# Optimization experiments

Hardware: AMD Instinct MI355X
Metric: run time of the kernel (lower is better)

## Reference

```python
import jax, jax.numpy as jnp
import numpy as np

WS = 25          # window_size
THRESHOLD = 3.5  # default threshold in find_low_quality_regions


def _conv1d_gelu(x, w, b, pad):
    # x: (N, C_in, L), w: (C_out, C_in, K) -> gelu(conv(x) + b), SAME length
    y = jax.lax.conv_general_dilated(
        x, w, window_strides=(1,), padding=[(pad, pad)],
        dimension_numbers=("NCH", "OIH", "NCH"))
    return jax.nn.gelu(y + b[None, :, None], approximate=False)


def setup_inputs() -> dict:
    key = jax.random.key(0)
    ks = jax.random.split(key, 12)
    B, T, D, H = 8, 25000, 256, 128
    s = 0.05
    return {
        "latents": jax.random.normal(ks[0], (B, T, D), jnp.float32),
        "conv0_w": jax.random.normal(ks[1], (H, D, 7), jnp.float32) * s,
        "conv0_b": jax.random.normal(ks[2], (H,), jnp.float32) * s,
        "conv1_w": jax.random.normal(ks[3], (H, H, 5), jnp.float32) * s,
        "conv1_b": jax.random.normal(ks[4], (H,), jnp.float32) * s,
        "conv2_w": jax.random.normal(ks[5], (H, H, 5), jnp.float32) * s,
        "conv2_b": jax.random.normal(ks[6], (H,), jnp.float32) * s,
        "head_w1": jax.random.normal(ks[7], (H, H), jnp.float32) * s,
        "head_b1": jax.random.normal(ks[8], (H,), jnp.float32) * s,
        "head_w2": jax.random.normal(ks[9], (1, H), jnp.float32) * s,
        "head_b2": jax.random.normal(ks[10], (1,), jnp.float32) * s,
    }


def reference(latents, conv0_w, conv0_b, conv1_w, conv1_b, conv2_w, conv2_b,
              head_w1, head_b1, head_w2, head_b2):
    B, T, D = latents.shape
    nw = (T - WS) // WS + 1  # number of non-overlapping windows
    # (B, nw, WS, D) -> (B*nw, D, WS): batch all windows through the critic
    x = latents[:, :nw * WS].reshape(B, nw, WS, D).reshape(B * nw, WS, D)
    x = jnp.transpose(x, (0, 2, 1))  # NCH
    x = _conv1d_gelu(x, conv0_w, conv0_b, pad=3)
    x = _conv1d_gelu(x, conv1_w, conv1_b, pad=2)
    x = _conv1d_gelu(x, conv2_w, conv2_b, pad=2)
    feat = x.mean(axis=2)  # AdaptiveAvgPool1d(1) -> (B*nw, H)
    h = jax.nn.gelu(feat @ head_w1.T + head_b1, approximate=False)
    score = jax.nn.sigmoid(h @ head_w2.T + head_b2)[:, 0] * 5.0  # (B*nw,)
    scores = score.reshape(B, nw).mean(axis=0)  # critic(window).mean() per window
    low_quality = scores < THRESHOLD  # windows the loop would append as regions
    return scores, low_quality
```

## Files before the change

### kernel.cpp

```cpp
#include <hip/hip_runtime.h>
#include <math.h>

#define BATCH 8
#define T_LEN 25000
#define NW    1000
#define WS    25
#define D0    256
#define H     128

typedef __bf16 bf16;
typedef bf16 bf16x8 __attribute__((ext_vector_type(8)));
typedef bf16 bf16x4 __attribute__((ext_vector_type(4)));
typedef float f32x4 __attribute__((ext_vector_type(4)));

__device__ __forceinline__ float gelu_fast(float x) {
    float y = 0.7978845608f * x * (1.0f + 0.044715f * x * x);
    float e = __expf(2.0f * y);
    float t = 1.0f - 2.0f * __builtin_amdgcn_rcpf(e + 1.0f);
    return 0.5f * x * (1.0f + t);
}

__global__ void repack_w(const float* __restrict__ w, bf16* __restrict__ dst,
                         int Cin, int K, int KSn, int total) {
    int t = blockIdx.x * 256 + threadIdx.x;
    if (t >= total) return;
    int j    = t & 7;
    int lane = (t >> 3) & 63;
    int mt   = (t >> 9) & 7;
    int ks   = (t >> 12) % KSn;
    int k    = t / (4096 * KSn);
    int m = lane & 15, q = lane >> 4;
    int co = mt * 16 + m;
    int ci = ks * 32 + q * 8 + j;
    dst[t] = (bf16)w[(co * Cin + ci) * K + k];
}

__global__ void cvt_bf16(const float* __restrict__ w, bf16* __restrict__ dst, int n) {
    int t = blockIdx.x * 256 + threadIdx.x;
    if (t < n) dst[t] = (bf16)w[t];
}

#define XT_LD 264
#define A_LD  136
#define OFF_A1   16896
#define OFF_FEAT 24784
#define OFF_H    25296
#define SMEM_BYTES 27200

__global__ __launch_bounds__(256, 6)
void critic_kernel(const float* __restrict__ lat,
                   const bf16* __restrict__ p0, const float* __restrict__ b0,
                   const bf16* __restrict__ p1, const float* __restrict__ b1,
                   const bf16* __restrict__ p2, const float* __restrict__ b2,
                   const bf16* __restrict__ hw1b, const float* __restrict__ hb1,
                   const float* __restrict__ hw2, const float* __restrict__ hb2,
                   float* __restrict__ scores_tmp) {
    __shared__ __align__(16) char smem[SMEM_BYTES];
    bf16  (*xT)[XT_LD]  = (bf16(*)[XT_LD])smem;
    bf16  (*a2T)[A_LD]  = (bf16(*)[A_LD])smem;
    bf16  (*a1T)[A_LD]  = (bf16(*)[A_LD])(smem + OFF_A1);
    float* feat = (float*)(smem + OFF_FEAT);
    float* hbuf = (float*)(smem + OFF_H);

    const int tid = threadIdx.x;
    const int bx  = blockIdx.x;
    const int b   = bx / NW;
    const int w   = bx % NW;

    {
        const float4* src4 = (const float4*)(lat + ((size_t)b * T_LEN + (size_t)w * WS) * D0);
        #pragma unroll
        for (int it = 0; it < 7; ++it) {
            int g = tid + it * 256;
            if (g < 1600) {
                int l = g >> 6, c0 = (g & 63) * 4;
                float4 v = src4[g];
                bf16x4 o = {(bf16)v.x, (bf16)v.y, (bf16)v.z, (bf16)v.w};
                *(bf16x4*)&xT[l + 3][c0] = o;
            }
        }
        bf16x4 z4 = {};
        #pragma unroll
        for (int it = 0; it < 2; ++it) {
            int i = tid + it * 256;
            if (i < 448) {
                int rr = i >> 6;
                int r = (rr < 3) ? rr : rr + 25;
                *(bf16x4*)&xT[r][(i & 63) * 4] = z4;
            }
        }
        {
            if (tid < 128) {
                int rr = tid >> 5;
                int r = (rr < 2) ? rr : rr + 25;
                *(bf16x4*)&a1T[r][(tid & 31) * 4] = z4;
            }
        }
    }
    __syncthreads();

    const int lane = tid & 63, wv = tid >> 6;
    const int m = lane & 15, q = lane >> 4;
    const bf16* xbase  = &xT[m][q * 8];
    const bf16* a1base = &a1T[m][q * 8];

    f32x4 acc[2][2] = {};
    {
        const bf16x8* A = (const bf16x8*)p0 + (size_t)wv * 64 + lane;
        #pragma unroll
        for (int k = 0; k < 7; ++k) {
            #pragma unroll
            for (int ks = 0; ks < 8; ++ks) {
                bf16x8 a0 = A[(k * 8 + ks) * 512];
                bf16x8 a1 = A[(k * 8 + ks) * 512 + 256];
                bf16x8 bb0 = *(const bf16x8*)(xbase + k * XT_LD + ks * 32);
                bf16x8 bb1 = *(const bf16x8*)(xbase + k * XT_LD + ks * 32 + 16 * XT_LD);
                acc[0][0] = __builtin_amdgcn_mfma_f32_16x16x32_bf16(a0, bb0, acc[0][0], 0, 0, 0);
                acc[0][1] = __builtin_amdgcn_mfma_f32_16x16x32_bf16(a0, bb1, acc[0][1], 0, 0, 0);
                acc[1][0] = __builtin_amdgcn_mfma_f32_16x16x32_bf16(a1, bb0, acc[1][0], 0, 0, 0);
                acc[1][1] = __builtin_amdgcn_mfma_f32_16x16x32_bf16(a1, bb1, acc[1][1], 0, 0, 0);
            }
        }
    }
    __syncthreads();
    {
        bf16x4 z4 = {};
        if (tid < 128) {
            int rr = tid >> 5;
            int r = (rr < 2) ? rr : rr + 25;
            *(bf16x4*)&a2T[r][(tid & 31) * 4] = z4;
        }
    }
    #pragma unroll
    for (int mt = 0; mt < 2; ++mt) {
        int co0 = (wv + 4 * mt) * 16 + q * 4;
        f32x4 bv = *(const f32x4*)&b0[co0];
        #pragma unroll
        for (int nt = 0; nt < 2; ++nt) {
            int l = nt * 16 + m;
            if (l < 25) {
                bf16x4 v;
                #pragma unroll
                for (int r = 0; r < 4; ++r)
                    v[r] = (bf16)gelu_fast(acc[mt][nt][r] + bv[r]);
                *(bf16x4*)&a1T[l + 2][co0] = v;
            }
        }
    }
    __syncthreads();

    f32x4 c1[2][2] = {};
    {
        const bf16x8* A = (const bf16x8*)p1 + (size_t)wv * 64 + lane;
        #pragma unroll
        for (int k = 0; k < 5; ++k) {
            #pragma unroll
            for (int ks = 0; ks < 4; ++ks) {
                bf16x8 a0 = A[(k * 4 + ks) * 512];
                bf16x8 a1 = A[(k * 4 + ks) * 512 + 256];
                bf16x8 bb0 = *(const bf16x8*)(a1base + k * A_LD + ks * 32);
                bf16x8 bb1 = *(const bf16x8*)(a1base + k * A_LD + ks * 32 + 16 * A_LD);
                c1[0][0] = __builtin_amdgcn_mfma_f32_16x16x32_bf16(a0, bb0, c1[0][0], 0, 0, 0);
                c1[0][1] = __builtin_amdgcn_mfma_f32_16x16x32_bf16(a0, bb1, c1[0][1], 0, 0, 0);
                c1[1][0] = __builtin_amdgcn_mfma_f32_16x16x32_bf16(a1, bb0, c1[1][0], 0, 0, 0);
                c1[1][1] = __builtin_amdgcn_mfma_f32_16x16x32_bf16(a1, bb1, c1[1][1], 0, 0, 0);
            }
        }
    }
    #pragma unroll
    for (int mt = 0; mt < 2; ++mt) {
        int co0 = (wv + 4 * mt) * 16 + q * 4;
        f32x4 bv = *(const f32x4*)&b1[co0];
        #pragma unroll
        for (int nt = 0; nt < 2; ++nt) {
            int l = nt * 16 + m;
            if (l < 25) {
                bf16x4 v;
                #pragma unroll
                for (int r = 0; r < 4; ++r)
                    v[r] = (bf16)gelu_fast(c1[mt][nt][r] + bv[r]);
                *(bf16x4*)&a2T[l + 2][co0] = v;
            }
        }
    }
    __syncthreads();

    f32x4 c2[2][2] = {};
    {
        const bf16* a2base = &a2T[m][q * 8];
        const bf16x8* A = (const bf16x8*)p2 + (size_t)wv * 64 + lane;
        #pragma unroll
        for (int k = 0; k < 5; ++k) {
            #pragma unroll
            for (int ks = 0; ks < 4; ++ks) {
                bf16x8 a0 = A[(k * 4 + ks) * 512];
                bf16x8 a1 = A[(k * 4 + ks) * 512 + 256];
                bf16x8 bb0 = *(const bf16x8*)(a2base + k * A_LD + ks * 32);
                bf16x8 bb1 = *(const bf16x8*)(a2base + k * A_LD + ks * 32 + 16 * A_LD);
                c2[0][0] = __builtin_amdgcn_mfma_f32_16x16x32_bf16(a0, bb0, c2[0][0], 0, 0, 0);
                c2[0][1] = __builtin_amdgcn_mfma_f32_16x16x32_bf16(a0, bb1, c2[0][1], 0, 0, 0);
                c2[1][0] = __builtin_amdgcn_mfma_f32_16x16x32_bf16(a1, bb0, c2[1][0], 0, 0, 0);
                c2[1][1] = __builtin_amdgcn_mfma_f32_16x16x32_bf16(a1, bb1, c2[1][1], 0, 0, 0);
            }
        }
    }
    #pragma unroll
    for (int mt = 0; mt < 2; ++mt) {
        int co0 = (wv + 4 * mt) * 16 + q * 4;
        f32x4 bv = *(const f32x4*)&b2[co0];
        f32x4 pool;
        #pragma unroll
        for (int r = 0; r < 4; ++r) {
            float s = gelu_fast(c2[mt][0][r] + bv[r]);
            float g1 = gelu_fast(c2[mt][1][r] + bv[r]);
            s += (m < 9) ? g1 : 0.0f;
            s += __shfl_xor(s, 1);
            s += __shfl_xor(s, 2);
            s += __shfl_xor(s, 4);
            s += __shfl_xor(s, 8);
            pool[r] = s * 0.04f;
        }
        if (m == 0) *(f32x4*)&feat[co0] = pool;
    }
    __syncthreads();

    if (tid < H) {
        const bf16x8* row = (const bf16x8*)(hw1b + tid * H);
        float a = hb1[tid];
        #pragma unroll
        for (int jv = 0; jv < 16; ++jv) {
            bf16x8 w8 = row[jv];
            #pragma unroll
            for (int u = 0; u < 8; ++u)
                a += (float)w8[u] * feat[jv * 8 + u];
        }
        hbuf[tid] = gelu_fast(a);
    }
    __syncthreads();

    if (tid < 64) {
        float p = hw2[tid] * hbuf[tid] + hw2[tid + 64] * hbuf[tid + 64];
        #pragma unroll
        for (int off = 32; off > 0; off >>= 1) p += __shfl_down(p, off);
        if (tid == 0) {
            float z = p + hb2[0];
            scores_tmp[bx] = 5.0f / (1.0f + expf(-z));
        }
    }
}

__global__ void finalize_kernel(const float* __restrict__ tmp, float* __restrict__ out) {
    int w = blockIdx.x * 256 + threadIdx.x;
    if (w < NW) {
        float s = 0.0f;
        #pragma unroll
        for (int b = 0; b < BATCH; ++b) s += tmp[b * NW + w];
        s *= 0.125f;
        out[w] = s;
        out[NW + w] = (s < 3.5f) ? 1.0f : 0.0f;
    }
}

extern "C" void kernel_launch(void* const* d_in, const int* in_sizes, int n_in,
                              void* d_out, int out_size, void* d_ws, size_t ws_size,
                              hipStream_t stream) {
    const float* lat  = (const float*)d_in[0];
    const float* c0w  = (const float*)d_in[1];
    const float* c0b  = (const float*)d_in[2];
    const float* c1w  = (const float*)d_in[3];
    const float* c1b  = (const float*)d_in[4];
    const float* c2w  = (const float*)d_in[5];
    const float* c2b  = (const float*)d_in[6];
    const float* hw1  = (const float*)d_in[7];
    const float* hb1  = (const float*)d_in[8];
    const float* hw2  = (const float*)d_in[9];
    const float* hb2  = (const float*)d_in[10];

    bf16* p0   = (bf16*)d_ws;
    bf16* p1   = (bf16*)((char*)d_ws + 458752);
    bf16* p2   = (bf16*)((char*)d_ws + 622592);
    bf16* hw1b = (bf16*)((char*)d_ws + 786432);
    float* tmp = (float*)((char*)d_ws + 819200);

    const int n0 = 128 * 256 * 7;
    const int n1 = 128 * 128 * 5;
    repack_w<<<(n0 + 255) / 256, 256, 0, stream>>>(c0w, p0, 256, 7, 8, n0);
    repack_w<<<(n1 + 255) / 256, 256, 0, stream>>>(c1w, p1, 128, 5, 4, n1);
    repack_w<<<(n1 + 255) / 256, 256, 0, stream>>>(c2w, p2, 128, 5, 4, n1);
    cvt_bf16<<<64, 256, 0, stream>>>(hw1, hw1b, 128 * 128);

    critic_kernel<<<BATCH * NW, 256, 0, stream>>>(lat, p0, c0b, p1, c1b, p2, c2b,
                                                  hw1b, hb1, hw2, hb2, tmp);
    finalize_kernel<<<4, 256, 0, stream>>>(tmp, (float*)d_out);
}
```

Before: 537.6 us.

## Process two windows per block to reuse weight fragments across more MFMAs

Each block now handles two adjacent windows, so every weight fragment loaded from global memory feeds twice as many MFMAs. Accumulator tiles double, shared memory roughly doubles, and the grid is halved. The launch-bounds occupancy hint drops from 6 to 3, trading occupancy and latency hiding for lower weight-load traffic per window.

Measured after the change: 504.5 us. 6.2% less time.

```diff
diff --git a/kernel.cpp b/kernel.cpp
--- a/kernel.cpp
+++ b/kernel.cpp
@@ -42,12 +42,12 @@
 
 #define XT_LD 264
 #define A_LD  136
-#define OFF_A1   16896
-#define OFF_FEAT 24784
-#define OFF_H    25296
-#define SMEM_BYTES 27200
-
-__global__ __launch_bounds__(256, 6)
+#define OFF_A1   32736
+#define OFF_FEAT 48512
+#define OFF_H    49536
+#define SMEM_BYTES 50560
+
+__global__ __launch_bounds__(256, 3)
 void critic_kernel(const float* __restrict__ lat,
                    const bf16* __restrict__ p0, const float* __restrict__ b0,
                    const bf16* __restrict__ p1, const float* __restrict__ b1,
@@ -64,47 +64,55 @@
 
     const int tid = threadIdx.x;
     const int bx  = blockIdx.x;
-    const int b   = bx / NW;
-    const int w   = bx % NW;
-
-    {
-        const float4* src4 = (const float4*)(lat + ((size_t)b * T_LEN + (size_t)w * WS) * D0);
-        #pragma unroll
-        for (int it = 0; it < 7; ++it) {
+    const int b   = bx / (NW / 2);
+    const int wi  = bx % (NW / 2);
+    const int w0  = 2 * wi;
+
+    {
+        const float4* src4 = (const float4*)(lat + ((size_t)b * T_LEN + (size_t)w0 * WS) * D0);
+        #pragma unroll
+        for (int it = 0; it < 12; ++it) {
             int g = tid + it * 256;
-            if (g < 1600) {
+            int l = g >> 6, c0 = (g & 63) * 4;
+            int r = (l < 25) ? (l + 3) : (l + 9);
+            float4 v = src4[g];
+            bf16x4 o = {(bf16)v.x, (bf16)v.y, (bf16)v.z, (bf16)v.w};
+            *(bf16x4*)&xT[r][c0] = o;
+        }
+        {
+            if (tid < 128) {
+                int g = 3072 + tid;
                 int l = g >> 6, c0 = (g & 63) * 4;
+                int r = (l < 25) ? (l + 3) : (l + 9);
                 float4 v = src4[g];
                 bf16x4 o = {(bf16)v.x, (bf16)v.y, (bf16)v.z, (bf16)v.w};
-                *(bf16x4*)&xT[l + 3][c0] = o;
+                *(bf16x4*)&xT[r][c0] = o;
             }
         }
         bf16x4 z4 = {};
         #pragma unroll
-        for (int it = 0; it < 2; ++it) {
+        for (int it = 0; it < 3; ++it) {
             int i = tid + it * 256;
-            if (i < 448) {
+            if (i < 768) {
                 int rr = i >> 6;
-                int r = (rr < 3) ? rr : rr + 25;
+                int r = (rr < 3) ? rr : ((rr < 9) ? rr + 25 : rr + 50);
                 *(bf16x4*)&xT[r][(i & 63) * 4] = z4;
             }
         }
-        {
-            if (tid < 128) {
-                int rr = tid >> 5;
-                int r = (rr < 2) ? rr : rr + 25;
-                *(bf16x4*)&a1T[r][(tid & 31) * 4] = z4;
-            }
+        if (tid < 256) {
+            int rr = tid >> 5;
+            int r = (rr < 2) ? rr : ((rr < 6) ? rr + 25 : rr + 50);
+            *(bf16x4*)&a1T[r][(tid & 31) * 4] = z4;
         }
     }
     __syncthreads();
 
     const int lane = tid & 63, wv = tid >> 6;
     const int m = lane & 15, q = lane >> 4;
-    const bf16* xbase  = &xT[m][q * 8];
-    const bf16* a1base = &a1T[m][q * 8];
-
-    f32x4 acc[2][2] = {};
+    const bf16* xb  = &xT[m][q * 8];
+    const bf16* a1b = &a1T[m][q * 8];
+
+    f32x4 acc[2][4] = {};
     {
         const bf16x8* A = (const bf16x8*)p0 + (size_t)wv * 64 + lane;
         #pragma unroll
@@ -113,43 +121,48 @@
             for (int ks = 0; ks < 8; ++ks) {
                 bf16x8 a0 = A[(k * 8 + ks) * 512];
                 bf16x8 a1 = A[(k * 8 + ks) * 512 + 256];
-                bf16x8 bb0 = *(const bf16x8*)(xbase + k * XT_LD + ks * 32);
-                bf16x8 bb1 = *(const bf16x8*)(xbase + k * XT_LD + ks * 32 + 16 * XT_LD);
+                const bf16* pB = xb + k * XT_LD + ks * 32;
+                bf16x8 bb0 = *(const bf16x8*)(pB);
+                bf16x8 bb1 = *(const bf16x8*)(pB + 16 * XT_LD);
+                bf16x8 bb2 = *(const bf16x8*)(pB + 31 * XT_LD);
+                bf16x8 bb3 = *(const bf16x8*)(pB + 47 * XT_LD);
                 acc[0][0] = __builtin_amdgcn_mfma_f32_16x16x32_bf16(a0, bb0, acc[0][0], 0, 0, 0);
                 acc[0][1] = __builtin_amdgcn_mfma_f32_16x16x32_bf16(a0, bb1, acc[0][1], 0, 0, 0);
+                acc[0][2] = __builtin_amdgcn_mfma_f32_16x16x32_bf16(a0, bb2, acc[0][2], 0, 0, 0);
+                acc[0][3] = __builtin_amdgcn_mfma_f32_16x16x32_bf16(a0, bb3, acc[0][3], 0, 0, 0);
                 acc[1][0] = __builtin_amdgcn_mfma_f32_16x16x32_bf16(a1, bb0, acc[1][0], 0, 0, 0);
                 acc[1][1] = __builtin_amdgcn_mfma_f32_16x16x32_bf16(a1, bb1, acc[1][1], 0, 0, 0);
+                acc[1][2] = __builtin_amdgcn_mfma_f32_16x16x32_bf16(a1, bb2, acc[1][2], 0, 0, 0);
+                acc[1][3] = __builtin_amdgcn_mfma_f32_16x16x32_bf16(a1, bb3, acc[1][3], 0, 0, 0);
             }
         }
     }
     __syncthreads();
     {
         bf16x4 z4 = {};
-        if (tid < 128) {
-            int rr = tid >> 5;
-            int r = (rr < 2) ? rr : rr + 25;
-            *(bf16x4*)&a2T[r][(tid & 31) * 4] = z4;
-        }
+        int rr = tid >> 5;
+        int r = (rr < 2) ? rr : ((rr < 6) ? rr + 25 : rr + 50);
+        *(bf16x4*)&a2T[r][(tid & 31) * 4] = z4;
     }
     #pragma unroll
     for (int mt = 0; mt < 2; ++mt) {
         int co0 = (wv + 4 * mt) * 16 + q * 4;
         f32x4 bv = *(const f32x4*)&b0[co0];
         #pragma unroll
-        for (int nt = 0; nt < 2; ++nt) {
-            int l = nt * 16 + m;
+        for (int nt = 0; nt < 4; ++nt) {
+            int l = (nt & 1) * 16 + m;
             if (l < 25) {
                 bf16x4 v;
                 #pragma unroll
                 for (int r = 0; r < 4; ++r)
                     v[r] = (bf16)gelu_fast(acc[mt][nt][r] + bv[r]);
-                *(bf16x4*)&a1T[l + 2][co0] = v;
-            }
-        }
-    }
-    __syncthreads();
-
-    f32x4 c1[2][2] = {};
+                *(bf16x4*)&a1T[l + 2 + 29 * (nt >> 1)][co0] = v;
+            }
+        }
+    }
+    __syncthreads();
+
+    f32x4 c1[2][4] = {};
     {
         const bf16x8* A = (const bf16x8*)p1 + (size_t)wv * 64 + lane;
         #pragma unroll
@@ -158,12 +171,19 @@
             for (int ks = 0; ks < 4; ++ks) {
                 bf16x8 a0 = A[(k * 4 + ks) * 512];
                 bf16x8 a1 = A[(k * 4 + ks) * 512 + 256];
-                bf16x8 bb0 = *(const bf16x8*)(a1base + k * A_LD + ks * 32);
-                bf16x8 bb1 = *(const bf16x8*)(a1base + k * A_LD + ks * 32 + 16 * A_LD);
+                const bf16* pB = a1b + k * A_LD + ks * 32;
+                bf16x8 bb0 = *(const bf16x8*)(pB);
+                bf16x8 bb1 = *(const bf16x8*)(pB + 16 * A_LD);
+                bf16x8 bb2 = *(const bf16x8*)(pB + 29 * A_LD);
+                bf16x8 bb3 = *(const bf16x8*)(pB + 45 * A_LD);
                 c1[0][0] = __builtin_amdgcn_mfma_f32_16x16x32_bf16(a0, bb0, c1[0][0], 0, 0, 0);
                 c1[0][1] = __builtin_amdgcn_mfma_f32_16x16x32_bf16(a0, bb1, c1[0][1], 0, 0, 0);
+                c1[0][2] = __builtin_amdgcn_mfma_f32_16x16x32_bf16(a0, bb2, c1[0][2], 0, 0, 0);
+                c1[0][3] = __builtin_amdgcn_mfma_f32_16x16x32_bf16(a0, bb3, c1[0][3], 0, 0, 0);
                 c1[1][0] = __builtin_amdgcn_mfma_f32_16x16x32_bf16(a1, bb0, c1[1][0], 0, 0, 0);
                 c1[1][1] = __builtin_amdgcn_mfma_f32_16x16x32_bf16(a1, bb1, c1[1][1], 0, 0, 0);
+                c1[1][2] = __builtin_amdgcn_mfma_f32_16x16x32_bf16(a1, bb2, c1[1][2], 0, 0, 0);
+                c1[1][3] = __builtin_amdgcn_mfma_f32_16x16x32_bf16(a1, bb3, c1[1][3], 0, 0, 0);
             }
         }
     }
@@ -172,22 +192,22 @@
         int co0 = (wv + 4 * mt) * 16 + q * 4;
         f32x4 bv = *(const f32x4*)&b1[co0];
         #pragma unroll
-        for (int nt = 0; nt < 2; ++nt) {
-            int l = nt * 16 + m;
+        for (int nt = 0; nt < 4; ++nt) {
+            int l = (nt & 1) * 16 + m;
             if (l < 25) {
                 bf16x4 v;
                 #pragma unroll
                 for (int r = 0; r < 4; ++r)
                     v[r] = (bf16)gelu_fast(c1[mt][nt][r] + bv[r]);
-                *(bf16x4*)&a2T[l + 2][co0] = v;
-            }
-        }
-    }
-    __syncthreads();
-
-    f32x4 c2[2][2] = {};
-    {
-        const bf16* a2base = &a2T[m][q * 8];
+                *(bf16x4*)&a2T[l + 2 + 29 * (nt >> 1)][co0] = v;
+            }
+        }
+    }
+    __syncthreads();
+
+    f32x4 c2[2][4] = {};
+    {
+        const bf16* a2b = &a2T[m][q * 8];
         const bf16x8* A = (const bf16x8*)p2 + (size_t)wv * 64 + lane;
         #pragma unroll
         for (int k = 0; k < 5; ++k) {
@@ -195,12 +215,19 @@
             for (int ks = 0; ks < 4; ++ks) {
                 bf16x8 a0 = A[(k * 4 + ks) * 512];
                 bf16x8 a1 = A[(k * 4 + ks) * 512 + 256];
-                bf16x8 bb0 = *(const bf16x8*)(a2base + k * A_LD + ks * 32);
-                bf16x8 bb1 = *(const bf16x8*)(a2base + k * A_LD + ks * 32 + 16 * A_LD);
+                const bf16* pB = a2b + k * A_LD + ks * 32;
+                bf16x8 bb0 = *(const bf16x8*)(pB);
+                bf16x8 bb1 = *(const bf16x8*)(pB + 16 * A_LD);
+                bf16x8 bb2 = *(const bf16x8*)(pB + 29 * A_LD);
+                bf16x8 bb3 = *(const bf16x8*)(pB + 45 * A_LD);
                 c2[0][0] = __builtin_amdgcn_mfma_f32_16x16x32_bf16(a0, bb0, c2[0][0], 0, 0, 0);
                 c2[0][1] = __builtin_amdgcn_mfma_f32_16x16x32_bf16(a0, bb1, c2[0][1], 0, 0, 0);
+                c2[0][2] = __builtin_amdgcn_mfma_f32_16x16x32_bf16(a0, bb2, c2[0][2], 0, 0, 0);
+                c2[0][3] = __builtin_amdgcn_mfma_f32_16x16x32_bf16(a0, bb3, c2[0][3], 0, 0, 0);
                 c2[1][0] = __builtin_amdgcn_mfma_f32_16x16x32_bf16(a1, bb0, c2[1][0], 0, 0, 0);
                 c2[1][1] = __builtin_amdgcn_mfma_f32_16x16x32_bf16(a1, bb1, c2[1][1], 0, 0, 0);
+                c2[1][2] = __builtin_amdgcn_mfma_f32_16x16x32_bf16(a1, bb2, c2[1][2], 0, 0, 0);
+                c2[1][3] = __builtin_amdgcn_mfma_f32_16x16x32_bf16(a1, bb3, c2[1][3], 0, 0, 0);
             }
         }
     }
@@ -208,43 +235,50 @@
     for (int mt = 0; mt < 2; ++mt) {
         int co0 = (wv + 4 * mt) * 16 + q * 4;
         f32x4 bv = *(const f32x4*)&b2[co0];
-        f32x4 pool;
-        #pragma unroll
-        for (int r = 0; r < 4; ++r) {
-            float s = gelu_fast(c2[mt][0][r] + bv[r]);
-            float g1 = gelu_fast(c2[mt][1][r] + bv[r]);
-            s += (m < 9) ? g1 : 0.0f;
-            s += __shfl_xor(s, 1);
-            s += __shfl_xor(s, 2);
-            s += __shfl_xor(s, 4);
-            s += __shfl_xor(s, 8);
-            pool[r] = s * 0.04f;
-        }
-        if (m == 0) *(f32x4*)&feat[co0] = pool;
-    }
-    __syncthreads();
-
-    if (tid < H) {
-        const bf16x8* row = (const bf16x8*)(hw1b + tid * H);
-        float a = hb1[tid];
+        #pragma unroll
+        for (int win = 0; win < 2; ++win) {
+            f32x4 pool;
+            #pragma unroll
+            for (int r = 0; r < 4; ++r) {
+                float s  = gelu_fast(c2[mt][2 * win][r] + bv[r]);
+                float g1 = gelu_fast(c2[mt][2 * win + 1][r] + bv[r]);
+                s += (m < 9) ? g1 : 0.0f;
+                s += __shfl_xor(s, 1);
+                s += __shfl_xor(s, 2);
+                s += __shfl_xor(s, 4);
+                s += __shfl_xor(s, 8);
+                pool[r] = s * 0.04f;
+            }
+            if (m == 0) *(f32x4*)&feat[win * 128 + co0] = pool;
+        }
+    }
+    __syncthreads();
+
+    {
+        int win = tid >> 7, co = tid & 127;
+        const bf16x8* row = (const bf16x8*)(hw1b + co * H);
+        const float* f = feat + win * 128;
+        float a = hb1[co];
         #pragma unroll
         for (int jv = 0; jv < 16; ++jv) {
             bf16x8 w8 = row[jv];
             #pragma unroll
             for (int u = 0; u < 8; ++u)
-                a += (float)w8[u] * feat[jv * 8 + u];
+                a += (float)w8[u] * f[jv * 8 + u];
         }
         hbuf[tid] = gelu_fast(a);
     }
     __syncthreads();
 
-    if (tid < 64) {
-        float p = hw2[tid] * hbuf[tid] + hw2[tid + 64] * hbuf[tid + 64];
+    if (tid < 128) {
+        int win = tid >> 6, j = tid & 63;
+        const float* hb = hbuf + win * 128;
+        float p = hw2[j] * hb[j] + hw2[j + 64] * hb[j + 64];
         #pragma unroll
         for (int off = 32; off > 0; off >>= 1) p += __shfl_down(p, off);
-        if (tid == 0) {
+        if (j == 0) {
             float z = p + hb2[0];
-            scores_tmp[bx] = 5.0f / (1.0f + expf(-z));
+            scores_tmp[b * NW + w0 + win] = 5.0f / (1.0f + expf(-z));
         }
     }
 }
@@ -289,7 +323,7 @@
     repack_w<<<(n1 + 255) / 256, 256, 0, stream>>>(c2w, p2, 128, 5, 4, n1);
     cvt_bf16<<<64, 256, 0, stream>>>(hw1, hw1b, 128 * 128);
 
-    critic_kernel<<<BATCH * NW, 256, 0, stream>>>(lat, p0, c0b, p1, c1b, p2, c2b,
-                                                  hw1b, hb1, hw2, hb2, tmp);
+    critic_kernel<<<BATCH * (NW / 2), 256, 0, stream>>>(lat, p0, c0b, p1, c1b, p2, c2b,
+                                                        hw1b, hb1, hw2, hb2, tmp);
     finalize_kernel<<<4, 256, 0, stream>>>(tmp, (float*)d_out);
 }
```
